# Performance work log

Hardware: AMD Instinct MI355X
Metric: run time of the kernel (lower is better)

## Reference

```python
import jax, jax.numpy as jnp
from jax import lax
import numpy as np

IMG = 1024          # original image H = W
HD = WD = 256       # detection feature map (stride 4)
CD = 128            # detection feature channels
HS = WS = 512       # segmentation feature map (stride 2)
CS = 32             # segmentation feature channels
FC = 1024           # detection head conv / fc filters
K = 2000            # pre-NMS topk
MAX_OUT = 500       # max proposals after NMS
NMS_THR = 1.0       # distance threshold in detection-grid units
CROP = 48           # instance crop size (instance_crop_size // 2)
CI = 64             # instance conv channels


def _conv(x, w, b):
    # x: [H,W,Cin] single map -> same-padded conv
    y = lax.conv_general_dilated(x[None], w, (1, 1), 'SAME',
                                 dimension_numbers=('NHWC', 'HWIO', 'NHWC'))[0]
    return y + b


def _conv_b(x, w, b):
    # x: [N,H,W,Cin] batched conv
    y = lax.conv_general_dilated(x, w, (1, 1), 'SAME',
                                 dimension_numbers=('NHWC', 'HWIO', 'NHWC'))
    return y + b


def setup_inputs() -> dict:
    key = jax.random.key(0)
    ks = jax.random.split(key, 10)
    s = 0.02
    return {
        'detection_features': jax.random.normal(ks[0], (HD, WD, CD), jnp.float32),
        'segmentation_features': jax.random.normal(ks[1], (HS, WS, CS), jnp.float32),
        'Wc': jax.random.normal(ks[2], (3, 3, CD, FC), jnp.float32) * s,
        'bc': jnp.zeros((FC,), jnp.float32),
        'Wfc': jax.random.normal(ks[3], (1, 1, FC, FC), jnp.float32) * s,
        'bfc': jnp.zeros((FC,), jnp.float32),
        'Ws': jax.random.normal(ks[4], (1, 1, FC, 1), jnp.float32) * s,
        'bs': jnp.zeros((1,), jnp.float32),
        'Wr': jax.random.normal(ks[5], (1, 1, FC, 2), jnp.float32) * s,
        'br': jnp.zeros((2,), jnp.float32),
        'Wi': jax.random.normal(ks[6], (3, 3, CS, CI), jnp.float32) * s,
        'bi': jnp.zeros((CI,), jnp.float32),
        'Wo': jax.random.normal(ks[7], (3, 3, CI, 1), jnp.float32) * s,
        'bo': jnp.zeros((1,), jnp.float32),
    }


def _forward(detection_features, segmentation_features,
             Wc, bc, Wfc, bfc, Ws, bs, Wr, br, Wi, bi, Wo, bo):
    x = jax.nn.relu(_conv(detection_features, Wc, bc))
    x = jax.nn.relu(_conv(x, Wfc, bfc))
    scores = jax.nn.sigmoid(_conv(x, Ws, bs))[..., 0]          # [HD,WD]
    reg = _conv(x, Wr, br)                                      # [HD,WD,2] offsets in grid units

    # ---- proposal_locations: decode, topk, distance-threshold NMS ----
    yy, xx = jnp.meshgrid(jnp.arange(HD, dtype=jnp.float32),
                          jnp.arange(WD, dtype=jnp.float32), indexing='ij')
    ctr = jnp.stack([yy, xx], axis=-1) + 0.5                    # cell centers
    locs = (ctr + reg) / jnp.array([HD, WD], jnp.float32)       # normalized [0,1]
    flat_scores = scores.reshape(-1)                            # [HD*WD]
    flat_locs = locs.reshape(-1, 2)

    top_s, top_i = lax.top_k(flat_scores, K)                    # pre-NMS topk (sorted desc)
    cand = flat_locs[top_i]                                     # [K,2] normalized

    grid_xy = cand * jnp.array([HD, WD], jnp.float32)           # grid-unit coords
    d2 = jnp.sum((grid_xy[:, None, :] - grid_xy[None, :, :]) ** 2, axis=-1)  # [K,K]
    close = d2 < (NMS_THR * NMS_THR)
    later = jnp.arange(K)[None, :] > jnp.arange(K)[:, None]

    def nms_body(i, suppressed):
        keep_i = jnp.logical_not(suppressed[i])
        return suppressed | (keep_i & close[i] & later[i])

    suppressed = lax.fori_loop(0, K, nms_body, jnp.zeros((K,), jnp.bool_))
    masked = jnp.where(suppressed, -1.0, top_s)
    proposed_scores, sel = lax.top_k(masked, MAX_OUT)           # [500]
    sel_norm = cand[sel]                                        # [500,2]
    decoded = sel_norm * jnp.float32(IMG)                       # pixel coords

    # ---- instance head: crop stride-2 seg features around each proposal ----
    seg_loc = decoded / 2.0
    start = jnp.clip(jnp.round(seg_loc - CROP / 2), 0, HS - CROP).astype(jnp.int32)  # [500,2]

    def crop_one(st):
        return lax.dynamic_slice(segmentation_features, (st[0], st[1], 0), (CROP, CROP, CS))

    crops = jax.vmap(crop_one)(start)                           # [500,48,48,CS]
    h = jax.nn.relu(_conv_b(crops, Wi, bi))                     # [500,48,48,CI]
    instance_output = jax.nn.sigmoid(_conv_b(h, Wo, bo))        # [500,48,48,1]

    cy, cx = jnp.meshgrid(jnp.arange(CROP), jnp.arange(CROP), indexing='ij')
    instance_coords = start[:, None, None, :] + jnp.stack([cy, cx], axis=-1)[None]  # [500,48,48,2]

    return proposed_scores, decoded, instance_output, instance_coords


def reference(detection_features, segmentation_features,
              Wc, bc, Wfc, bfc, Ws, bs, Wr, br, Wi, bi, Wo, bo):
    return _forward(detection_features, segmentation_features,
                    Wc, bc, Wfc, bfc, Ws, bs, Wr, br, Wi, bi, Wo, bo)
```

## Files before the change

kernel.cpp:

```cpp
#include <hip/hip_runtime.h>
#include <math.h>

#define KTOP 2000
#define MAXOUT 500
#define CANDCAP 4096
#define NSEL 3600
#define RC2 16

typedef __attribute__((ext_vector_type(8))) short short8;
typedef __attribute__((ext_vector_type(4))) float f32x4;
typedef __attribute__((ext_vector_type(4))) double f64x4;

__device__ __forceinline__ unsigned short f2bf(float f) {
  unsigned int u = __float_as_uint(f);
  unsigned int r = ((u >> 16) & 1u) + 0x7FFFu;
  return (unsigned short)((u + r) >> 16);
}

__global__ __launch_bounds__(256) void transpose_bf16_kernel(
    const float* __restrict__ W, unsigned short* __restrict__ WT, int K, int N)
{
  __shared__ float t[32][33];
  const int k0 = blockIdx.x << 5, n0 = blockIdx.y << 5;
  const int tid = threadIdx.x;
  const int r = tid >> 5, c = tid & 31;
#pragma unroll
  for (int p = 0; p < 4; ++p)
    t[r + (p << 3)][c] = W[(size_t)(k0 + r + (p << 3)) * N + n0 + c];
  __syncthreads();
#pragma unroll
  for (int p = 0; p < 4; ++p)
    WT[(size_t)(n0 + r + (p << 3)) * K + k0 + c] = f2bf(t[c][r + (p << 3)]);
}

__global__ __launch_bounds__(256) void prep_wib_kernel(
    const float* __restrict__ Wi, unsigned short* __restrict__ WiB)
{
  const int t = blockIdx.x * 256 + threadIdx.x;
  if (t < 9 * 64 * 32) {
    const int tap = t / 2048, r = t & 2047, co = r >> 5, ci = r & 31;
    WiB[t] = f2bf(Wi[((size_t)tap * 32 + ci) * 64 + co]);
  }
}

__global__ __launch_bounds__(256) void pad_df_bf16(
    const float* __restrict__ df, unsigned short* __restrict__ dfb)
{
  const int t = blockIdx.x * 256 + threadIdx.x;
  if (t >= 258 * 258 * 16) return;
  const int p = t >> 4;
  const int c8 = (t & 15) << 3;
  const int gy = p / 258 - 1, gx = p % 258 - 1;
  uint4 out = make_uint4(0, 0, 0, 0);
  if (gy >= 0 && gy < 256 && gx >= 0 && gx < 256) {
    const float* src = &df[((size_t)(gy * 256 + gx)) * 128 + c8];
    const float4 v0 = *(const float4*)src;
    const float4 v1 = *(const float4*)(src + 4);
    out.x = (unsigned int)f2bf(v0.x) | ((unsigned int)f2bf(v0.y) << 16);
    out.y = (unsigned int)f2bf(v0.z) | ((unsigned int)f2bf(v0.w) << 16);
    out.z = (unsigned int)f2bf(v1.x) | ((unsigned int)f2bf(v1.y) << 16);
    out.w = (unsigned int)f2bf(v1.z) | ((unsigned int)f2bf(v1.w) << 16);
  }
  *(uint4*)&dfb[(size_t)p * 128 + c8] = out;
}

__global__ __launch_bounds__(256) void conv1_mfma(
    const unsigned short* __restrict__ dfb, const unsigned short* __restrict__ WcT,
    const float* __restrict__ bc, unsigned short* __restrict__ x1b, int pt0)
{
  __shared__ __align__(16) unsigned short smem[2 * 128 * 64];
  unsigned short* As = smem;
  unsigned short* Bs = smem + 128 * 64;
  const int tid = threadIdx.x;
  const int n0 = blockIdx.x << 7;
  const int m0 = blockIdx.y << 7;
  const int Pbase = (pt0 << 6) + m0;
  const int ybase = Pbase >> 8, x0 = Pbase & 255;
  const int wv = tid >> 6, lane = tid & 63;
  const int wm = (wv & 1) << 6, wn = (wv >> 1) << 6;
  const int l15 = lane & 15, quad = lane >> 4;

  const int tr = tid >> 3;
  const int g8 = tid & 7;
  const int xg = ((g8 ^ (tr & 7)) << 4);
  int koff[2];
#pragma unroll
  for (int s = 0; s < 2; ++s)
    koff[s] = ((((s << 2) + quad) ^ (l15 & 7)) << 3);

  f32x4 acc[4][4];
  const f32x4 z4 = {0.f, 0.f, 0.f, 0.f};
#pragma unroll
  for (int i = 0; i < 4; ++i)
#pragma unroll
    for (int j = 0; j < 4; ++j) acc[i][j] = z4;

  for (int kc = 0; kc < 18; ++kc) {
    const int tap = kc >> 1, ci0 = (kc & 1) << 6;
    const int dy = tap / 3 - 1, dx = tap % 3 - 1;
    const size_t abase =
        ((size_t)((ybase + dy + 1) * 258 + (x0 + dx + 1))) * 128 + ci0;
#pragma unroll
    for (int p = 0; p < 4; ++p) {
      const int r = (p << 5) + tr;
      __builtin_amdgcn_global_load_lds(
          (const unsigned int*)((const char*)&dfb[abase + (size_t)r * 128] + xg),
          (unsigned int*)&As[(r << 6) + (g8 << 3)], 16, 0, 0);
    }
#pragma unroll
    for (int p = 0; p < 4; ++p) {
      const int n = (p << 5) + tr;
      __builtin_amdgcn_global_load_lds(
          (const unsigned int*)((const char*)&WcT[(size_t)(n0 + n) * 1152 + (kc << 6)] + xg),
          (unsigned int*)&Bs[(n << 6) + (g8 << 3)], 16, 0, 0);
    }
    __syncthreads();
#pragma unroll
    for (int s = 0; s < 2; ++s) {
      short8 a[4], b[4];
#pragma unroll
      for (int i = 0; i < 4; ++i)
        a[i] = *(short8*)&As[((wm + (i << 4) + l15) << 6) + koff[s]];
#pragma unroll
      for (int j = 0; j < 4; ++j)
        b[j] = *(short8*)&Bs[((wn + (j << 4) + l15) << 6) + koff[s]];
#pragma unroll
      for (int i = 0; i < 4; ++i)
#pragma unroll
        for (int j = 0; j < 4; ++j)
          acc[i][j] = __builtin_amdgcn_mfma_f32_16x16x32_bf16(a[i], b[j], acc[i][j], 0, 0, 0);
    }
    __syncthreads();
  }
#pragma unroll
  for (int i = 0; i < 4; ++i)
#pragma unroll
    for (int j = 0; j < 4; ++j) {
      const int col = wn + (j << 4) + l15;
      const float bb = bc[n0 + col];
#pragma unroll
      for (int rg = 0; rg < 4; ++rg) {
        const int row = wm + (i << 4) + (quad << 2) + rg;
        const float v = fmaxf(acc[i][j][rg] + bb, 0.f);
        x1b[(size_t)(m0 + row) * 1024 + n0 + col] = f2bf(v);
      }
    }
}

__global__ __launch_bounds__(256) void fc_mfma(
    const unsigned short* __restrict__ x1b, const unsigned short* __restrict__ WfcT,
    const float* __restrict__ bfc, const float* __restrict__ Wsc,
    float* __restrict__ part, int pt0)
{
  __shared__ __align__(16) unsigned short smem[2 * 128 * 64];
  unsigned short* As = smem;
  unsigned short* Bs = smem + 128 * 64;
  const int tid = threadIdx.x;
  const int n0 = blockIdx.x << 7;
  const int m0 = blockIdx.y << 7;
  const int Pbase = (pt0 << 6) + m0;
  const int wv = tid >> 6, lane = tid & 63;
  const int wm = (wv & 1) << 6, wn = (wv >> 1) << 6;
  const int l15 = lane & 15, quad = lane >> 4;

  const int tr = tid >> 3;
  const int g8 = tid & 7;
  const int xg = ((g8 ^ (tr & 7)) << 4);
  int koff[2];
#pragma unroll
  for (int s = 0; s < 2; ++s)
    koff[s] = ((((s << 2) + quad) ^ (l15 & 7)) << 3);

  f32x4 acc[4][4];
  const f32x4 z4 = {0.f, 0.f, 0.f, 0.f};
#pragma unroll
  for (int i = 0; i < 4; ++i)
#pragma unroll
    for (int j = 0; j < 4; ++j) acc[i][j] = z4;

  for (int kc = 0; kc < 16; ++kc) {
#pragma unroll
    for (int p = 0; p < 4; ++p) {
      const int r = (p << 5) + tr;
      __builtin_amdgcn_global_load_lds(
          (const unsigned int*)((const char*)&x1b[(size_t)(m0 + r) * 1024 + (kc << 6)] + xg),
          (unsigned int*)&As[(r << 6) + (g8 << 3)], 16, 0, 0);
    }
#pragma unroll
    for (int p = 0; p < 4; ++p) {
      const int n = (p << 5) + tr;
      __builtin_amdgcn_global_load_lds(
          (const unsigned int*)((const char*)&WfcT[(size_t)(n0 + n) * 1024 + (kc << 6)] + xg),
          (unsigned int*)&Bs[(n << 6) + (g8 << 3)], 16, 0, 0);
    }
    __syncthreads();
#pragma unroll
    for (int s = 0; s < 2; ++s) {
      short8 a[4], b[4];
#pragma unroll
      for (int i = 0; i < 4; ++i)
        a[i] = *(short8*)&As[((wm + (i << 4) + l15) << 6) + koff[s]];
#pragma unroll
      for (int j = 0; j < 4; ++j)
        b[j] = *(short8*)&Bs[((wn + (j << 4) + l15) << 6) + koff[s]];
#pragma unroll
      for (int i = 0; i < 4; ++i)
#pragma unroll
        for (int j = 0; j < 4; ++j)
          acc[i][j] = __builtin_amdgcn_mfma_f32_16x16x32_bf16(a[i], b[j], acc[i][j], 0, 0, 0);
    }
    __syncthreads();
  }
  float wsv[4], bfv[4];
#pragma unroll
  for (int j = 0; j < 4; ++j) {
    const int col = n0 + wn + (j << 4) + l15;
    wsv[j] = Wsc[col];
    bfv[j] = bfc[col];
  }
  float* red = (float*)smem;
#pragma unroll
  for (int i = 0; i < 4; ++i)
#pragma unroll
    for (int rg = 0; rg < 4; ++rg) {
      const int row = wm + (i << 4) + (quad << 2) + rg;
      float ps = 0.f;
#pragma unroll
      for (int j = 0; j < 4; ++j) {
        const float v = fmaxf(acc[i][j][rg] + bfv[j], 0.f);
        ps = fmaf(v, wsv[j], ps);
      }
      red[row * 33 + ((wv >> 1) << 4) + l15] = ps;
    }
  __syncthreads();
  if (tid < 128) {
    float s = 0.f;
#pragma unroll
    for (int sl = 0; sl < 32; ++sl) s += red[tid * 33 + sl];
    part[(size_t)blockIdx.x * 65536 + Pbase + tid] = s;
  }
}

__global__ __launch_bounds__(256) void head_finalize_kernel(
    const float* __restrict__ part, const float* __restrict__ bs,
    float* __restrict__ scores)
{
  const int pix = blockIdx.x * 256 + threadIdx.x;
  float s = 0.f;
#pragma unroll
  for (int cb = 0; cb < 8; ++cb) s += part[(size_t)cb * 65536 + pix];
  s += bs[0];
  scores[pix] = 1.f / (1.f + expf(-s));
}

__global__ __launch_bounds__(1024) void select_kernel(
    const float* __restrict__ scores, unsigned int* __restrict__ cand_idx,
    unsigned int* __restrict__ cand_cnt)
{
  __shared__ unsigned int hist[256];
  __shared__ unsigned int sh_prefix;
  __shared__ int scan_s[1024];
  const int tid = threadIdx.x;

  unsigned int prefix = 0u;
  int need = NSEL;
  for (int byte = 3; byte >= 0; --byte) {
    if (tid < 256) hist[tid] = 0u;
    __syncthreads();
    const int sh = byte * 8;
    const unsigned int mhi = (byte == 3) ? 0u : (0xFFFFFFFFu << (sh + 8));
    for (int i = tid; i < 65536; i += 1024) {
      const unsigned int b = __float_as_uint(scores[i]);
      if ((b & mhi) == prefix) atomicAdd(&hist[(b >> sh) & 255u], 1u);
    }
    __syncthreads();
    if (tid == 0) {
      int cum = 0;
      for (int v = 255; v >= 0; --v) {
        const int c = (int)hist[v];
        if (cum + c >= need) { sh_prefix = prefix | ((unsigned)v << sh); break; }
        cum += c;
      }
      hist[0] = (unsigned int)cum;
    }
    __syncthreads();
    prefix = sh_prefix;
    need -= (int)hist[0];
    __syncthreads();
  }
  const float thr = __uint_as_float(prefix);

  const int b0 = tid << 6;
  int my = 0;
  for (int k = 0; k < 64; ++k)
    if (scores[b0 + k] >= thr) ++my;
  scan_s[tid] = my;
  __syncthreads();
  for (int off = 1; off < 1024; off <<= 1) {
    const int a = scan_s[tid];
    const int b = (tid >= off) ? scan_s[tid - off] : 0;
    __syncthreads();
    scan_s[tid] = a + b;
    __syncthreads();
  }
  int pos = scan_s[tid] - my;
  const int total = scan_s[1023];
  for (int k = 0; k < 64; ++k) {
    if (scores[b0 + k] >= thr) {
      if (pos < CANDCAP) cand_idx[pos] = (unsigned int)(b0 + k);
      ++pos;
    }
  }
  if (tid == 0)
    *cand_cnt = (unsigned int)(total > CANDCAP ? CANDCAP : total);
}

#define PSTR 133
__global__ __launch_bounds__(512) void rescore_conv(
    const float* __restrict__ df, const float* __restrict__ Wc,
    const float* __restrict__ bc,
    const unsigned int* __restrict__ cand_idx,
    const unsigned int* __restrict__ cand_cnt,
    double* __restrict__ x1g)
{
  __shared__ double patt[16 * PSTR];
  __shared__ int rrs[16], ccs[16];
  const int cnt = (int)*cand_cnt;
  const int c0 = blockIdx.x * RC2;
  if (c0 >= cnt) return;
  const int tid = threadIdx.x;
  const int wv = tid >> 6, lane = tid & 63;
  const int m = lane & 15, quad = lane >> 4;
  const int co_base = wv << 7;

  if (tid < 16) {
    const int slot = (c0 + tid < cnt) ? c0 + tid : c0;
    const unsigned int idx = cand_idx[slot];
    rrs[tid] = (int)(idx >> 8); ccs[tid] = (int)(idx & 255u);
  }

  f64x4 acc[8];
  const f64x4 z4 = {0.0, 0.0, 0.0, 0.0};
#pragma unroll
  for (int t = 0; t < 8; ++t) acc[t] = z4;

  for (int tap = 0; tap < 9; ++tap) {
    const int dy = tap / 3 - 1, dx = tap % 3 - 1;
    __syncthreads();
    for (int p = tid; p < 2048; p += 512) {
      const int c = p >> 7, ci = p & 127;
      const int gy = rrs[c] + dy, gx = ccs[c] + dx;
      float v = 0.f;
      if (gy >= 0 && gy < 256 && gx >= 0 && gx < 256)
        v = df[((size_t)((gy << 8) + gx)) * 128 + ci];
      patt[c * PSTR + ci] = (double)v;
    }
    __syncthreads();
    const float* wrow = &Wc[(size_t)(tap * 128 + quad) * 1024 + co_base + m];
    float wf[8];
#pragma unroll
    for (int t = 0; t < 8; ++t) wf[t] = wrow[t << 4];
    for (int k4 = 0; k4 < 32; ++k4) {
      float wn[8];
      if (k4 + 1 < 32) {
#pragma unroll
        for (int t = 0; t < 8; ++t)
          wn[t] = wrow[(size_t)((k4 + 1) << 2) * 1024 + (t << 4)];
      }
      const double a = patt[m * PSTR + (k4 << 2) + quad];
#pragma unroll
      for (int t = 0; t < 8; ++t)
        acc[t] = __builtin_amdgcn_mfma_f64_16x16x4f64(a, (double)wf[t], acc[t], 0, 0, 0);
      if (k4 + 1 < 32) {
#pragma unroll
        for (int t = 0; t < 8; ++t) wf[t] = wn[t];
      }
    }
  }
#pragma unroll
  for (int t = 0; t < 8; ++t) {
    const int co = co_base + (t << 4) + m;
    const double bb = (double)bc[co];
#pragma unroll
    for (int rg = 0; rg < 4; ++rg) {
      const int cand = (quad << 2) + rg;
      if (c0 + cand < cnt) {
        const double v = acc[t][rg] + bb;
        x1g[(size_t)(c0 + cand) * 1024 + co] = v > 0.0 ? v : 0.0;
      }
    }
  }
}

__global__ __launch_bounds__(512) void rescore_fc(
    const double* __restrict__ x1g, const float* __restrict__ Wfc,
    const float* __restrict__ bfc, const float* __restrict__ Wsc,
    const float* __restrict__ bs, const float* __restrict__ Wrg,
    const float* __restrict__ br,
    const unsigned int* __restrict__ cand_cnt,
    unsigned long long* __restrict__ cand_sb,
    double* __restrict__ cand_ry, double* __restrict__ cand_rx)
{
  __shared__ double xbuf[16 * PSTR];
  __shared__ double partw[3][8][16];
  const int cnt = (int)*cand_cnt;
  const int c0 = blockIdx.x * RC2;
  if (c0 >= cnt) return;
  const int tid = threadIdx.x;
  const int wv = tid >> 6, lane = tid & 63;
  const int m = lane & 15, quad = lane >> 4;
  const int co_base = wv << 7;

  f64x4 acc[8];
  const f64x4 z4 = {0.0, 0.0, 0.0, 0.0};
#pragma unroll
  for (int t = 0; t < 8; ++t) acc[t] = z4;

  for (int kc = 0; kc < 8; ++kc) {
    __syncthreads();
    for (int p = tid; p < 2048; p += 512) {
      const int c = p >> 7, k = p & 127;
      const int row = (c0 + c < cnt) ? c0 + c : c0;
      xbuf[c * PSTR + k] = x1g[(size_t)row * 1024 + (kc << 7) + k];
    }
    __syncthreads();
    const float* wrow = &Wfc[(size_t)((kc << 7) + quad) * 1024 + co_base + m];
    float wf[8];
#pragma unroll
    for (int t = 0; t < 8; ++t) wf[t] = wrow[t << 4];
    for (int k4 = 0; k4 < 32; ++k4) {
      float wn[8];
      if (k4 + 1 < 32) {
#pragma unroll
        for (int t = 0; t < 8; ++t)
          wn[t] = wrow[(size_t)((k4 + 1) << 2) * 1024 + (t << 4)];
      }
      const double a = xbuf[m * PSTR + (k4 << 2) + quad];
#pragma unroll
      for (int t = 0; t < 8; ++t)
        acc[t] = __builtin_amdgcn_mfma_f64_16x16x4f64(a, (double)wf[t], acc[t], 0, 0, 0);
      if (k4 + 1 < 32) {
#pragma unroll
        for (int t = 0; t < 8; ++t) wf[t] = wn[t];
      }
    }
  }

  double ps[4] = {0, 0, 0, 0}, py[4] = {0, 0, 0, 0}, px[4] = {0, 0, 0, 0};
#pragma unroll
  for (int t = 0; t < 8; ++t) {
    const int co = co_base + (t << 4) + m;
    const double bfv = (double)bfc[co];
    const double wsv = (double)Wsc[co];
    const double w0 = (double)Wrg[co * 2], w1 = (double)Wrg[co * 2 + 1];
#pragma unroll
    for (int rg = 0; rg < 4; ++rg) {
      double v = acc[t][rg] + bfv;
      v = v > 0.0 ? v : 0.0;
      ps[rg] = fma(v, wsv, ps[rg]);
      py[rg] = fma(v, w0, py[rg]);
      px[rg] = fma(v, w1, px[rg]);
    }
  }
#pragma unroll
  for (int off = 1; off <= 8; off <<= 1) {
#pragma unroll
    for (int rg = 0; rg < 4; ++rg) {
      ps[rg] += __shfl_xor(ps[rg], off, 64);
      py[rg] += __shfl_xor(py[rg], off, 64);
      px[rg] += __shfl_xor(px[rg], off, 64);
    }
  }
  if (m == 0) {
#pragma unroll
    for (int rg = 0; rg < 4; ++rg) {
      const int cand = (quad << 2) + rg;
      partw[0][wv][cand] = ps[rg];
      partw[1][wv][cand] = py[rg];
      partw[2][wv][cand] = px[rg];
    }
  }
  __syncthreads();
  if (tid < 48) {
    const int cand = tid & 15, h = tid >> 4;
    double s = 0.0;
#pragma unroll
    for (int w8 = 0; w8 < 8; ++w8) s += partw[h][w8][cand];
    if (c0 + cand < cnt) {
      if (h == 0) {
        const double lg = s + (double)bs[0];
        const double sg = 1.0 / (1.0 + exp(-lg));
        cand_sb[c0 + cand] = (unsigned long long)__double_as_longlong(sg);
      } else if (h == 1) cand_ry[c0 + cand] = s + (double)br[0];
      else               cand_rx[c0 + cand] = s + (double)br[1];
    }
  }
}

__global__ __launch_bounds__(1024) void proposal_kernel(
    const unsigned int* __restrict__ cand_idx,
    const unsigned int* __restrict__ cand_cnt,
    const unsigned long long* __restrict__ cand_sb,
    const double* __restrict__ cand_ry, const double* __restrict__ cand_rx,
    unsigned int* __restrict__ cellrank, unsigned int* __restrict__ nbrg,
    double* __restrict__ cyg, double* __restrict__ cxg,
    int* __restrict__ startb, float* __restrict__ out_ps,
    float* __restrict__ out_dec)
{
  __shared__ unsigned long long sk[2048];
  __shared__ unsigned int si[2048];
  __shared__ unsigned int hist[256];
  __shared__ unsigned long long sh_pref;
  __shared__ unsigned char kept[2048];
  __shared__ unsigned char nbrc[2048];
  __shared__ int scan[2048];
  __shared__ volatile unsigned int changed;
  __shared__ int sh_maxreg;

  const int tid = threadIdx.x;
  const int cnt = (int)*cand_cnt;

  for (int i = tid; i < 65536; i += 1024) cellrank[i] = 0xFFFFFFFFu;

  unsigned long long prefix = 0ull;
  int need = KTOP;
  for (int byte = 7; byte >= 0; --byte) {
    if (tid < 256) hist[tid] = 0u;
    __syncthreads();
    const int sh = byte * 8;
    const unsigned long long mhi =
        (byte == 7) ? 0ull : (0xFFFFFFFFFFFFFFFFull << (sh + 8));
    for (int i = tid; i < cnt; i += 1024) {
      const unsigned long long k = cand_sb[i];
      if ((k & mhi) == prefix) atomicAdd(&hist[(unsigned int)((k >> sh) & 255u)], 1u);
    }
    __syncthreads();
    if (tid == 0) {
      int cum = 0;
      for (int v = 255; v >= 0; --v) {
        const int c = (int)hist[v];
        if (cum + c >= need) {
          sh_pref = prefix | ((unsigned long long)(unsigned)v << sh);
          break;
        }
// ... 227 lines not shown
      b[j] = *(const short8*)&WiB[((tap << 6) + (j << 4) + l15) * 32 + (quad << 3)];
#pragma unroll
    for (int i = 0; i < 6; ++i) {
      const short8 a = *(const short8*)&ins[(pbase[i] + off) * ISTR + (quad << 3)];
#pragma unroll
      for (int j = 0; j < 4; ++j)
        acc[i][j] = __builtin_amdgcn_mfma_f32_16x16x32_bf16(a, b[j], acc[i][j], 0, 0, 0);
    }
  }

  float bv[4];
#pragma unroll
  for (int j = 0; j < 4; ++j) bv[j] = bi[(j << 4) + l15];

  for (int half = 0; half < 2; ++half) {
    __syncthreads();
    if ((wv >> 1) == half) {
#pragma unroll
      for (int i = 0; i < 6; ++i)
#pragma unroll
        for (int j = 0; j < 4; ++j)
#pragma unroll
          for (int rg = 0; rg < 4; ++rg) {
            const int m = wmb + (i << 4) + (quad << 2) + rg;
            const int pp = m - half * 192;
            const float v = fmaxf(acc[i][j][rg] + bv[j], 0.f);
            ins[pp * 72 + (j << 4) + l15] = f2bf(v);
          }
    }
    __syncthreads();
    for (int t = tid; t < 192 * 8; t += 256) {
      const int pp = t >> 3, c8 = t & 7;
      const uint4 v = *(const uint4*)&ins[pp * 72 + (c8 << 3)];
      *(uint4*)&h[((size_t)li * 2304 + (tile * 384 + half * 192 + pp)) * 64 + (c8 << 3)] = v;
    }
  }
}

__global__ __launch_bounds__(256) void conv_o_kernel(
    const unsigned short* __restrict__ h, const float* __restrict__ Wo,
    const float* __restrict__ bo, const int* __restrict__ startb,
    float* __restrict__ out_io, float* __restrict__ out_ic, int inst0)
{
  __shared__ __align__(16) unsigned short hs[324 * 72];
  __shared__ float wos[576];
  const int li = blockIdx.y;
  const int inst = inst0 + li;
  const int tile = blockIdx.x;
  const int ty0 = (tile / 3) << 4;
  const int tx0 = (tile % 3) << 4;
  const int tid = threadIdx.x;

  for (int i = tid; i < 576; i += 256) wos[i] = Wo[i];
  for (int p = tid; p < 324; p += 256) {
    const int iy = p / 18, ix = p - iy * 18;
    const int gy = ty0 - 1 + iy, gx = tx0 - 1 + ix;
    unsigned short* dst = &hs[p * 72];
    if (gy >= 0 && gy < 48 && gx >= 0 && gx < 48) {
      const unsigned short* src = &h[((size_t)li * 2304 + gy * 48 + gx) * 64];
#pragma unroll
      for (int q = 0; q < 8; ++q) *(uint4*)&dst[q << 3] = *(const uint4*)&src[q << 3];
    } else {
#pragma unroll
      for (int q = 0; q < 8; ++q) *(uint4*)&dst[q << 3] = make_uint4(0, 0, 0, 0);
    }
  }
  __syncthreads();

  const int ly = tid >> 4, lx = tid & 15;
  float a = 0.f;
#pragma unroll
  for (int ky = 0; ky < 3; ++ky)
#pragma unroll
    for (int kx = 0; kx < 3; ++kx) {
      const unsigned short* hp = &hs[((ly + ky) * 18 + lx + kx) * 72];
      const float* wp = &wos[(ky * 3 + kx) << 6];
#pragma unroll
      for (int c8 = 0; c8 < 8; ++c8) {
        const uint4 hv = *(const uint4*)&hp[c8 << 3];
        const unsigned int uu[4] = {hv.x, hv.y, hv.z, hv.w};
#pragma unroll
        for (int e = 0; e < 4; ++e) {
          const float f0 = __uint_as_float(uu[e] << 16);
          const float f1 = __uint_as_float(uu[e] & 0xFFFF0000u);
          a = fmaf(f0, wp[(c8 << 3) + (e << 1)], a);
          a = fmaf(f1, wp[(c8 << 3) + (e << 1) + 1], a);
        }
      }
    }
  a += bo[0];
  const float o = 1.f / (1.f + expf(-a));
  const int gy = ty0 + ly, gx = tx0 + lx;
  const size_t p = ((size_t)inst * 48 + gy) * 48 + gx;
  out_io[p] = o;
  const int sy = startb[inst * 2], sx = startb[inst * 2 + 1];
  out_ic[p * 2]     = (float)(sy + gy);
  out_ic[p * 2 + 1] = (float)(sx + gx);
}

extern "C" void kernel_launch(void* const* d_in, const int* in_sizes, int n_in,
                              void* d_out, int out_size, void* d_ws, size_t ws_size,
                              hipStream_t stream)
{
  const float* df  = (const float*)d_in[0];
  const float* seg = (const float*)d_in[1];
  const float* Wc  = (const float*)d_in[2];
  const float* bc  = (const float*)d_in[3];
  const float* Wfc = (const float*)d_in[4];
  const float* bfc = (const float*)d_in[5];
  const float* Wsc = (const float*)d_in[6];
  const float* bs  = (const float*)d_in[7];
  const float* Wrg = (const float*)d_in[8];
  const float* br  = (const float*)d_in[9];
  const float* Wi  = (const float*)d_in[10];
  const float* bi  = (const float*)d_in[11];
  const float* Wo  = (const float*)d_in[12];
  const float* bo  = (const float*)d_in[13];

  const size_t SZ_WCT = 2359296ull, SZ_WFT = 2097152ull, SZ_WIB = 36864ull,
               SZ_DFB = 17040384ull,
               SZ_PART = 2097152ull, SZ_SC = 262144ull, SZ_CR = 262144ull,
               SZ_NB = 131072ull, SZ_STB = 4096ull, SZ_CI = CANDCAP * 4ull,
               SZ_SB = CANDCAP * 8ull, SZ_RY = CANDCAP * 8ull,
               SZ_RX = CANDCAP * 8ull, SZ_CY = 16384ull, SZ_CX = 16384ull,
               SZ_X1G = (size_t)CANDCAP * 1024ull * 8ull,
               SZ_CNT = 256ull;
  const size_t FIXED = SZ_WCT + SZ_WFT + SZ_WIB + SZ_DFB + SZ_PART + SZ_SC +
                       SZ_CR + SZ_NB + SZ_STB + SZ_CI + SZ_SB + SZ_RY + SZ_RX +
                       SZ_CY + SZ_CX + SZ_X1G + SZ_CNT;
  char* w = (char*)d_ws;
  size_t region = (ws_size > FIXED) ? ((ws_size - FIXED) & ~(size_t)255) : 0;
  char* fb = w + region;
  unsigned short* WcT = (unsigned short*)fb;   fb += SZ_WCT;
  unsigned short* WfcT = (unsigned short*)fb;  fb += SZ_WFT;
  unsigned short* WiB = (unsigned short*)fb;   fb += SZ_WIB;
  unsigned short* dfb = (unsigned short*)fb;   fb += SZ_DFB;
  float* part = (float*)fb;                    fb += SZ_PART;
  float* scores = (float*)fb;                  fb += SZ_SC;
  unsigned int* cellrank = (unsigned int*)fb;  fb += SZ_CR;
  unsigned int* nbrg = (unsigned int*)fb;      fb += SZ_NB;
  int* startb = (int*)fb;                      fb += SZ_STB;
  unsigned int* cand_idx = (unsigned int*)fb;  fb += SZ_CI;
  unsigned long long* cand_sb = (unsigned long long*)fb; fb += SZ_SB;
  double* cand_ry = (double*)fb;               fb += SZ_RY;
  double* cand_rx = (double*)fb;               fb += SZ_RX;
  double* cyg = (double*)fb;                   fb += SZ_CY;
  double* cxg = (double*)fb;                   fb += SZ_CX;
  double* x1g = (double*)fb;                   fb += SZ_X1G;
  unsigned int* cand_cnt = (unsigned int*)fb;
  unsigned short* x1b = (unsigned short*)w;
  unsigned short* hb = (unsigned short*)w;

  size_t tiles_fit = region / 131072ull;
  int pt_chunk = 2;
  while ((size_t)(pt_chunk * 2) <= tiles_fit && pt_chunk < 1024) pt_chunk <<= 1;
  size_t inst_fit = region / 294912ull;
  const int opts[12] = {500, 250, 125, 100, 50, 25, 20, 10, 5, 4, 2, 1};
  int inst_chunk = 1;
  for (int o = 0; o < 12; ++o)
    if ((size_t)opts[o] <= inst_fit) { inst_chunk = opts[o]; break; }

  float* out = (float*)d_out;
  float* out_ps  = out;
  float* out_dec = out + 500;
  float* out_io  = out + 1500;
  float* out_ic  = out + 1153500;

  transpose_bf16_kernel<<<dim3(36, 32), 256, 0, stream>>>(Wc, WcT, 1152, 1024);
  transpose_bf16_kernel<<<dim3(32, 32), 256, 0, stream>>>(Wfc, WfcT, 1024, 1024);
  prep_wib_kernel<<<72, 256, 0, stream>>>(Wi, WiB);
  pad_df_bf16<<<4161, 256, 0, stream>>>(df, dfb);

  for (int c = 0; c < 1024 / pt_chunk; ++c) {
    conv1_mfma<<<dim3(8, pt_chunk / 2), 256, 0, stream>>>(dfb, WcT, bc, x1b,
                                                          c * pt_chunk);
    fc_mfma<<<dim3(8, pt_chunk / 2), 256, 0, stream>>>(x1b, WfcT, bfc, Wsc,
                                                       part, c * pt_chunk);
  }
  head_finalize_kernel<<<256, 256, 0, stream>>>(part, bs, scores);
  select_kernel<<<1, 1024, 0, stream>>>(scores, cand_idx, cand_cnt);
  rescore_conv<<<CANDCAP / RC2, 512, 0, stream>>>(df, Wc, bc, cand_idx,
                                                  cand_cnt, x1g);
  rescore_fc<<<CANDCAP / RC2, 512, 0, stream>>>(x1g, Wfc, bfc, Wsc, bs, Wrg,
                                                br, cand_cnt, cand_sb,
                                                cand_ry, cand_rx);
  proposal_kernel<<<1, 1024, 0, stream>>>(cand_idx, cand_cnt, cand_sb, cand_ry,
                                          cand_rx, cellrank, nbrg, cyg, cxg,
                                          startb, out_ps, out_dec);
  for (int c = 0; c < 500 / inst_chunk; ++c) {
    conv_i_mfma<<<dim3(6, inst_chunk), 256, 0, stream>>>(seg, WiB, bi, startb,
                                                         hb, c * inst_chunk);
    conv_o_kernel<<<dim3(9, inst_chunk), 256, 0, stream>>>(hb, Wo, bo, startb,
                                                           out_io, out_ic,
                                                           c * inst_chunk);
  }
}
```

Measured before the change: 1.354 ms.

## Use 256x256 double-buffered MFMA GEMM tiles with phased compute and wider rescore

The conv1 and fc GEMMs move from 128x128 tiles with 256 threads to 256x256 tiles with 512 threads. Global-to-LDS loads are double-buffered and the MFMA work is split into barrier-separated phases with s_setprio, so loads overlap compute and each tile reuses more data. The fc epilogue now reduces with wave shuffles, and the number of partial-score slices drops from 8 to 4. rescore_conv now handles 32 candidates per block split across two column halves. The larger tiles use much more LDS and registers, which lowers occupancy, and they need a larger minimum chunk size.

Result: faster. 1.282 ms (-5.3%).

```diff
diff --git a/kernel.cpp b/kernel.cpp
--- a/kernel.cpp
+++ b/kernel.cpp
@@ -5,6 +5,7 @@
 #define MAXOUT 500
 #define CANDCAP 4096
 #define NSEL 3600
+#define RCC 32
 #define RC2 16
 
 typedef __attribute__((ext_vector_type(8))) short short8;
@@ -15,6 +16,19 @@
   unsigned int u = __float_as_uint(f);
   unsigned int r = ((u >> 16) & 1u) + 0x7FFFu;
   return (unsigned short)((u + r) >> 16);
+}
+
+__device__ __forceinline__ void ld_lds16(const void* g, void* l) {
+  __builtin_amdgcn_global_load_lds((const unsigned int*)g, (unsigned int*)l,
+                                   16, 0, 0);
+}
+
+__device__ __forceinline__ void hard_barrier() {
+  asm volatile("" ::: "memory");
+  __builtin_amdgcn_sched_barrier(0);
+  __builtin_amdgcn_s_barrier();
+  __builtin_amdgcn_sched_barrier(0);
+  asm volatile("" ::: "memory");
 }
 
 __global__ __launch_bounds__(256) void transpose_bf16_kernel(
@@ -64,179 +78,247 @@
   *(uint4*)&dfb[(size_t)p * 128 + c8] = out;
 }
 
-__global__ __launch_bounds__(256) void conv1_mfma(
+__device__ __forceinline__ void ktile_phases(
+    const unsigned short* __restrict__ A0, const unsigned short* __restrict__ B0,
+    const int arow, const int brow, const int ok0, const int ok1,
+    f32x4 (&acc)[8][4])
+{
+  short8 Af[4][2], Bf[2][2][2];
+#pragma unroll
+  for (int m = 0; m < 4; ++m) {
+    Af[m][0] = *(const short8*)&A0[((arow + (m << 4)) << 6) + ok0];
+    Af[m][1] = *(const short8*)&A0[((arow + (m << 4)) << 6) + ok1];
+  }
+#pragma unroll
+  for (int n = 0; n < 2; ++n) {
+    Bf[0][n][0] = *(const short8*)&B0[((brow + (n << 4)) << 6) + ok0];
+    Bf[0][n][1] = *(const short8*)&B0[((brow + (n << 4)) << 6) + ok1];
+  }
+  hard_barrier();
+  __builtin_amdgcn_s_setprio(1);
+#pragma unroll
+  for (int m = 0; m < 4; ++m)
+#pragma unroll
+    for (int n = 0; n < 2; ++n) {
+      acc[m][n] = __builtin_amdgcn_mfma_f32_16x16x32_bf16(Af[m][0], Bf[0][n][0], acc[m][n], 0, 0, 0);
+      acc[m][n] = __builtin_amdgcn_mfma_f32_16x16x32_bf16(Af[m][1], Bf[0][n][1], acc[m][n], 0, 0, 0);
+    }
+  __builtin_amdgcn_s_setprio(0);
+  hard_barrier();
+#pragma unroll
+  for (int n = 0; n < 2; ++n) {
+    Bf[1][n][0] = *(const short8*)&B0[((brow + ((n + 2) << 4)) << 6) + ok0];
+    Bf[1][n][1] = *(const short8*)&B0[((brow + ((n + 2) << 4)) << 6) + ok1];
+  }
+  hard_barrier();
+  __builtin_amdgcn_s_setprio(1);
+#pragma unroll
+  for (int m = 0; m < 4; ++m)
+#pragma unroll
+    for (int n = 0; n < 2; ++n) {
+      acc[m][n + 2] = __builtin_amdgcn_mfma_f32_16x16x32_bf16(Af[m][0], Bf[1][n][0], acc[m][n + 2], 0, 0, 0);
+      acc[m][n + 2] = __builtin_amdgcn_mfma_f32_16x16x32_bf16(Af[m][1], Bf[1][n][1], acc[m][n + 2], 0, 0, 0);
+    }
+  __builtin_amdgcn_s_setprio(0);
+  hard_barrier();
+#pragma unroll
+  for (int m = 0; m < 4; ++m) {
+    Af[m][0] = *(const short8*)&A0[((arow + 64 + (m << 4)) << 6) + ok0];
+    Af[m][1] = *(const short8*)&A0[((arow + 64 + (m << 4)) << 6) + ok1];
+  }
+  hard_barrier();
+  __builtin_amdgcn_s_setprio(1);
+#pragma unroll
+  for (int m = 0; m < 4; ++m)
+#pragma unroll
+    for (int n = 0; n < 2; ++n) {
+      acc[m + 4][n + 2] = __builtin_amdgcn_mfma_f32_16x16x32_bf16(Af[m][0], Bf[1][n][0], acc[m + 4][n + 2], 0, 0, 0);
+      acc[m + 4][n + 2] = __builtin_amdgcn_mfma_f32_16x16x32_bf16(Af[m][1], Bf[1][n][1], acc[m + 4][n + 2], 0, 0, 0);
+    }
+  __builtin_amdgcn_s_setprio(0);
+  hard_barrier();
+  __builtin_amdgcn_s_setprio(1);
+#pragma unroll
+  for (int m = 0; m < 4; ++m)
+#pragma unroll
+    for (int n = 0; n < 2; ++n) {
+      acc[m + 4][n] = __builtin_amdgcn_mfma_f32_16x16x32_bf16(Af[m][0], Bf[0][n][0], acc[m + 4][n], 0, 0, 0);
+      acc[m + 4][n] = __builtin_amdgcn_mfma_f32_16x16x32_bf16(Af[m][1], Bf[0][n][1], acc[m + 4][n], 0, 0, 0);
+    }
+  __builtin_amdgcn_s_setprio(0);
+  hard_barrier();
+}
+
+__global__ __launch_bounds__(512) void conv1_mfma(
     const unsigned short* __restrict__ dfb, const unsigned short* __restrict__ WcT,
     const float* __restrict__ bc, unsigned short* __restrict__ x1b, int pt0)
 {
-  __shared__ __align__(16) unsigned short smem[2 * 128 * 64];
-  unsigned short* As = smem;
-  unsigned short* Bs = smem + 128 * 64;
+  __shared__ __align__(16) unsigned short smem[65536];
   const int tid = threadIdx.x;
-  const int n0 = blockIdx.x << 7;
-  const int m0 = blockIdx.y << 7;
-  const int Pbase = (pt0 << 6) + m0;
-  const int ybase = Pbase >> 8, x0 = Pbase & 255;
   const int wv = tid >> 6, lane = tid & 63;
-  const int wm = (wv & 1) << 6, wn = (wv >> 1) << 6;
+  const int wr = wv >> 2, wc = wv & 3;
   const int l15 = lane & 15, quad = lane >> 4;
-
-  const int tr = tid >> 3;
-  const int g8 = tid & 7;
+  const int n0 = blockIdx.x << 8;
+  const int lm0 = blockIdx.y << 8;
+  const int Pbase = (pt0 << 6) + lm0;
+  const int y = Pbase >> 8;
+  const int tr = tid >> 3, g8 = tid & 7;
   const int xg = ((g8 ^ (tr & 7)) << 4);
-  int koff[2];
-#pragma unroll
-  for (int s = 0; s < 2; ++s)
-    koff[s] = ((((s << 2) + quad) ^ (l15 & 7)) << 3);
-
-  f32x4 acc[4][4];
+  const int axr = l15 & 7;
+  const int ok0 = ((quad ^ axr) << 3);
+  const int ok1 = (((4 + quad) ^ axr) << 3);
+  const int arow = (wr << 7) + l15;
+  const int brow = (wc << 6) + l15;
+
+  float bcv[4];
+#pragma unroll
+  for (int j = 0; j < 4; ++j) bcv[j] = bc[n0 + (wc << 6) + (j << 4) + l15];
+
+  f32x4 acc[8][4];
   const f32x4 z4 = {0.f, 0.f, 0.f, 0.f};
 #pragma unroll
-  for (int i = 0; i < 4; ++i)
+  for (int i = 0; i < 8; ++i)
 #pragma unroll
     for (int j = 0; j < 4; ++j) acc[i][j] = z4;
 
-  for (int kc = 0; kc < 18; ++kc) {
-    const int tap = kc >> 1, ci0 = (kc & 1) << 6;
+  const char* WB = (const char*)WcT + ((size_t)(n0 + tr) * 1152) * 2 + xg;
+  unsigned short* lA = &smem[(tr << 6) + (g8 << 3)];
+
+  auto issue = [&](int kt, int buf) {
+    const int tap = kt >> 1, ci0 = (kt & 1) << 6;
     const int dy = tap / 3 - 1, dx = tap % 3 - 1;
-    const size_t abase =
-        ((size_t)((ybase + dy + 1) * 258 + (x0 + dx + 1))) * 128 + ci0;
-#pragma unroll
-    for (int p = 0; p < 4; ++p) {
-      const int r = (p << 5) + tr;
-      __builtin_amdgcn_global_load_lds(
-          (const unsigned int*)((const char*)&dfb[abase + (size_t)r * 128] + xg),
-          (unsigned int*)&As[(r << 6) + (g8 << 3)], 16, 0, 0);
-    }
-#pragma unroll
-    for (int p = 0; p < 4; ++p) {
-      const int n = (p << 5) + tr;
-      __builtin_amdgcn_global_load_lds(
-          (const unsigned int*)((const char*)&WcT[(size_t)(n0 + n) * 1152 + (kc << 6)] + xg),
-          (unsigned int*)&Bs[(n << 6) + (g8 << 3)], 16, 0, 0);
-    }
-    __syncthreads();
-#pragma unroll
-    for (int s = 0; s < 2; ++s) {
-      short8 a[4], b[4];
-#pragma unroll
-      for (int i = 0; i < 4; ++i)
-        a[i] = *(short8*)&As[((wm + (i << 4) + l15) << 6) + koff[s]];
-#pragma unroll
-      for (int j = 0; j < 4; ++j)
-        b[j] = *(short8*)&Bs[((wn + (j << 4) + l15) << 6) + koff[s]];
-#pragma unroll
-      for (int i = 0; i < 4; ++i)
-#pragma unroll
-        for (int j = 0; j < 4; ++j)
-          acc[i][j] = __builtin_amdgcn_mfma_f32_16x16x32_bf16(a[i], b[j], acc[i][j], 0, 0, 0);
-    }
-    __syncthreads();
-  }
-#pragma unroll
-  for (int i = 0; i < 4; ++i)
-#pragma unroll
-    for (int j = 0; j < 4; ++j) {
-      const int col = wn + (j << 4) + l15;
-      const float bb = bc[n0 + col];
+    const char* Ab = (const char*)dfb +
+        (((size_t)((y + dy + 1) * 258 + dx + 1)) * 128 + ci0) * 2 +
+        (size_t)tr * 256 + xg;
+    unsigned short* la = lA + buf * 32768;
+    unsigned short* lb = la + 16384;
+    const char* Bb = WB + (size_t)kt * 128;
+#pragma unroll
+    for (int i = 0; i < 4; ++i)
+      ld_lds16(Ab + (size_t)i * 16384, la + i * 4096);
+#pragma unroll
+    for (int i = 0; i < 4; ++i)
+      ld_lds16(Bb + (size_t)i * 147456, lb + i * 4096);
+  };
+
+  issue(0, 0);
+  issue(1, 1);
+#pragma unroll 2
+  for (int kt = 0; kt < 18; ++kt) {
+    const int buf = kt & 1;
+    if (kt < 17) asm volatile("s_waitcnt vmcnt(8)" ::: "memory");
+    else         asm volatile("s_waitcnt vmcnt(0)" ::: "memory");
+    hard_barrier();
+    ktile_phases(&smem[buf * 32768], &smem[buf * 32768 + 16384],
+                 arow, brow, ok0, ok1, acc);
+    if (kt < 16) issue(kt + 2, buf);
+  }
+
+#pragma unroll
+  for (int m = 0; m < 8; ++m)
+#pragma unroll
+    for (int n = 0; n < 4; ++n) {
+      const int col = n0 + (wc << 6) + (n << 4) + l15;
+      const float bb = bcv[n];
 #pragma unroll
       for (int rg = 0; rg < 4; ++rg) {
-        const int row = wm + (i << 4) + (quad << 2) + rg;
-        const float v = fmaxf(acc[i][j][rg] + bb, 0.f);
-        x1b[(size_t)(m0 + row) * 1024 + n0 + col] = f2bf(v);
-      }
-    }
-}
-
-__global__ __launch_bounds__(256) void fc_mfma(
+        const int row = lm0 + (wr << 7) + (m << 4) + (quad << 2) + rg;
+        const float v = fmaxf(acc[m][n][rg] + bb, 0.f);
+        x1b[(size_t)row * 1024 + col] = f2bf(v);
+      }
+    }
+}
+
+__global__ __launch_bounds__(512) void fc_mfma(
     const unsigned short* __restrict__ x1b, const unsigned short* __restrict__ WfcT,
     const float* __restrict__ bfc, const float* __restrict__ Wsc,
     float* __restrict__ part, int pt0)
 {
-  __shared__ __align__(16) unsigned short smem[2 * 128 * 64];
-  unsigned short* As = smem;
-  unsigned short* Bs = smem + 128 * 64;
+  __shared__ __align__(16) unsigned short smem[65536];
   const int tid = threadIdx.x;
-  const int n0 = blockIdx.x << 7;
-  const int m0 = blockIdx.y << 7;
-  const int Pbase = (pt0 << 6) + m0;
   const int wv = tid >> 6, lane = tid & 63;
-  const int wm = (wv & 1) << 6, wn = (wv >> 1) << 6;
+  const int wr = wv >> 2, wc = wv & 3;
   const int l15 = lane & 15, quad = lane >> 4;
-
-  const int tr = tid >> 3;
-  const int g8 = tid & 7;
+  const int n0 = blockIdx.x << 8;
+  const int lm0 = blockIdx.y << 8;
+  const int Pbase = (pt0 << 6) + lm0;
+  const int tr = tid >> 3, g8 = tid & 7;
   const int xg = ((g8 ^ (tr & 7)) << 4);
-  int koff[2];
-#pragma unroll
-  for (int s = 0; s < 2; ++s)
-    koff[s] = ((((s << 2) + quad) ^ (l15 & 7)) << 3);
-
-  f32x4 acc[4][4];
-  const f32x4 z4 = {0.f, 0.f, 0.f, 0.f};
-#pragma unroll
-  for (int i = 0; i < 4; ++i)
-#pragma unroll
-    for (int j = 0; j < 4; ++j) acc[i][j] = z4;
-
-  for (int kc = 0; kc < 16; ++kc) {
-#pragma unroll
-    for (int p = 0; p < 4; ++p) {
-      const int r = (p << 5) + tr;
-      __builtin_amdgcn_global_load_lds(
-          (const unsigned int*)((const char*)&x1b[(size_t)(m0 + r) * 1024 + (kc << 6)] + xg),
-          (unsigned int*)&As[(r << 6) + (g8 << 3)], 16, 0, 0);
-    }
-#pragma unroll
-    for (int p = 0; p < 4; ++p) {
-      const int n = (p << 5) + tr;
-      __builtin_amdgcn_global_load_lds(
-          (const unsigned int*)((const char*)&WfcT[(size_t)(n0 + n) * 1024 + (kc << 6)] + xg),
-          (unsigned int*)&Bs[(n << 6) + (g8 << 3)], 16, 0, 0);
-    }
-    __syncthreads();
-#pragma unroll
-    for (int s = 0; s < 2; ++s) {
-      short8 a[4], b[4];
-#pragma unroll
-      for (int i = 0; i < 4; ++i)
-        a[i] = *(short8*)&As[((wm + (i << 4) + l15) << 6) + koff[s]];
-#pragma unroll
-      for (int j = 0; j < 4; ++j)
-        b[j] = *(short8*)&Bs[((wn + (j << 4) + l15) << 6) + koff[s]];
-#pragma unroll
-      for (int i = 0; i < 4; ++i)
-#pragma unroll
-        for (int j = 0; j < 4; ++j)
-          acc[i][j] = __builtin_amdgcn_mfma_f32_16x16x32_bf16(a[i], b[j], acc[i][j], 0, 0, 0);
-    }
-    __syncthreads();
-  }
+  const int axr = l15 & 7;
+  const int ok0 = ((quad ^ axr) << 3);
+  const int ok1 = (((4 + quad) ^ axr) << 3);
+  const int arow = (wr << 7) + l15;
+  const int brow = (wc << 6) + l15;
+
   float wsv[4], bfv[4];
 #pragma unroll
   for (int j = 0; j < 4; ++j) {
-    const int col = n0 + wn + (j << 4) + l15;
+    const int col = n0 + (wc << 6) + (j << 4) + l15;
     wsv[j] = Wsc[col];
     bfv[j] = bfc[col];
   }
+
+  f32x4 acc[8][4];
+  const f32x4 z4 = {0.f, 0.f, 0.f, 0.f};
+#pragma unroll
+  for (int i = 0; i < 8; ++i)
+#pragma unroll
+    for (int j = 0; j < 4; ++j) acc[i][j] = z4;
+
+  const char* AB = (const char*)x1b + ((size_t)(lm0 + tr) * 1024) * 2 + xg;
+  const char* WB = (const char*)WfcT + ((size_t)(n0 + tr) * 1024) * 2 + xg;
+  unsigned short* lA = &smem[(tr << 6) + (g8 << 3)];
+
+  auto issue = [&](int kt, int buf) {
+    unsigned short* la = lA + buf * 32768;
+    unsigned short* lb = la + 16384;
+    const char* Ab = AB + (size_t)kt * 128;
+    const char* Bb = WB + (size_t)kt * 128;
+#pragma unroll
+    for (int i = 0; i < 4; ++i)
+      ld_lds16(Ab + (size_t)i * 131072, la + i * 4096);
+#pragma unroll
+    for (int i = 0; i < 4; ++i)
+      ld_lds16(Bb + (size_t)i * 131072, lb + i * 4096);
+  };
+
+  issue(0, 0);
+  issue(1, 1);
+#pragma unroll 2
+  for (int kt = 0; kt < 16; ++kt) {
+    const int buf = kt & 1;
+    if (kt < 15) asm volatile("s_waitcnt vmcnt(8)" ::: "memory");
+    else         asm volatile("s_waitcnt vmcnt(0)" ::: "memory");
+    hard_barrier();
+    ktile_phases(&smem[buf * 32768], &smem[buf * 32768 + 16384],
+                 arow, brow, ok0, ok1, acc);
+    if (kt < 14) issue(kt + 2, buf);
+  }
+
   float* red = (float*)smem;
 #pragma unroll
-  for (int i = 0; i < 4; ++i)
+  for (int m = 0; m < 8; ++m)
 #pragma unroll
     for (int rg = 0; rg < 4; ++rg) {
-      const int row = wm + (i << 4) + (quad << 2) + rg;
       float ps = 0.f;
 #pragma unroll
-      for (int j = 0; j < 4; ++j) {
-        const float v = fmaxf(acc[i][j][rg] + bfv[j], 0.f);
-        ps = fmaf(v, wsv[j], ps);
-      }
-      red[row * 33 + ((wv >> 1) << 4) + l15] = ps;
-    }
-  __syncthreads();
-  if (tid < 128) {
+      for (int n = 0; n < 4; ++n) {
+        const float v = fmaxf(acc[m][n][rg] + bfv[n], 0.f);
+        ps = fmaf(v, wsv[n], ps);
+      }
+#pragma unroll
+      for (int off = 1; off <= 8; off <<= 1)
+        ps += __shfl_xor(ps, off, 64);
+      if (l15 == 0) {
+        const int row = (wr << 7) + (m << 4) + (quad << 2) + rg;
+        red[row * 5 + wc] = ps;
+      }
+    }
+  __syncthreads();
+  if (tid < 256) {
     float s = 0.f;
 #pragma unroll
-    for (int sl = 0; sl < 32; ++sl) s += red[tid * 33 + sl];
+    for (int w8 = 0; w8 < 4; ++w8) s += red[tid * 5 + w8];
     part[(size_t)blockIdx.x * 65536 + Pbase + tid] = s;
   }
 }
@@ -248,7 +330,7 @@
   const int pix = blockIdx.x * 256 + threadIdx.x;
   float s = 0.f;
 #pragma unroll
-  for (int cb = 0; cb < 8; ++cb) s += part[(size_t)cb * 65536 + pix];
+  for (int cb = 0; cb < 4; ++cb) s += part[(size_t)cb * 65536 + pix];
   s += bs[0];
   scores[pix] = 1.f / (1.f + expf(-s));
 }
@@ -323,31 +405,34 @@
     const unsigned int* __restrict__ cand_cnt,
     double* __restrict__ x1g)
 {
-  __shared__ double patt[16 * PSTR];
-  __shared__ int rrs[16], ccs[16];
+  __shared__ double patt[RCC * PSTR];
+  __shared__ int rrs[RCC], ccs[RCC];
   const int cnt = (int)*cand_cnt;
-  const int c0 = blockIdx.x * RC2;
+  const int nb = blockIdx.x & 1;
+  const int c0 = (blockIdx.x >> 1) * RCC;
   if (c0 >= cnt) return;
   const int tid = threadIdx.x;
   const int wv = tid >> 6, lane = tid & 63;
   const int m = lane & 15, quad = lane >> 4;
-  const int co_base = wv << 7;
-
-  if (tid < 16) {
+  const int co_base = (nb << 9) + (wv << 6);
+
+  if (tid < RCC) {
     const int slot = (c0 + tid < cnt) ? c0 + tid : c0;
     const unsigned int idx = cand_idx[slot];
     rrs[tid] = (int)(idx >> 8); ccs[tid] = (int)(idx & 255u);
   }
 
-  f64x4 acc[8];
+  f64x4 acc[2][4];
   const f64x4 z4 = {0.0, 0.0, 0.0, 0.0};
 #pragma unroll
-  for (int t = 0; t < 8; ++t) acc[t] = z4;
+  for (int ct = 0; ct < 2; ++ct)
+#pragma unroll
+    for (int t = 0; t < 4; ++t) acc[ct][t] = z4;
 
   for (int tap = 0; tap < 9; ++tap) {
     const int dy = tap / 3 - 1, dx = tap % 3 - 1;
     __syncthreads();
-    for (int p = tid; p < 2048; p += 512) {
+    for (int p = tid; p < RCC * 128; p += 512) {
       const int c = p >> 7, ci = p & 127;
       const int gy = rrs[c] + dy, gx = ccs[c] + dx;
       float v = 0.f;
@@ -357,39 +442,45 @@
     }
     __syncthreads();
     const float* wrow = &Wc[(size_t)(tap * 128 + quad) * 1024 + co_base + m];
-    float wf[8];
-#pragma unroll
-    for (int t = 0; t < 8; ++t) wf[t] = wrow[t << 4];
+    float wf[4];
+#pragma unroll
+    for (int t = 0; t < 4; ++t) wf[t] = wrow[t << 4];
     for (int k4 = 0; k4 < 32; ++k4) {
-      float wn[8];
+      float wn[4];
       if (k4 + 1 < 32) {
 #pragma unroll
-        for (int t = 0; t < 8; ++t)
+        for (int t = 0; t < 4; ++t)
           wn[t] = wrow[(size_t)((k4 + 1) << 2) * 1024 + (t << 4)];
       }
-      const double a = patt[m * PSTR + (k4 << 2) + quad];
-#pragma unroll
-      for (int t = 0; t < 8; ++t)
-        acc[t] = __builtin_amdgcn_mfma_f64_16x16x4f64(a, (double)wf[t], acc[t], 0, 0, 0);
+      const double a0 = patt[m * PSTR + (k4 << 2) + quad];
+      const double a1 = patt[(16 + m) * PSTR + (k4 << 2) + quad];
+#pragma unroll
+      for (int t = 0; t < 4; ++t)
+        acc[0][t] = __builtin_amdgcn_mfma_f64_16x16x4f64(a0, (double)wf[t], acc[0][t], 0, 0, 0);
+#pragma unroll
+      for (int t = 0; t < 4; ++t)
+        acc[1][t] = __builtin_amdgcn_mfma_f64_16x16x4f64(a1, (double)wf[t], acc[1][t], 0, 0, 0);
       if (k4 + 1 < 32) {
 #pragma unroll
-        for (int t = 0; t < 8; ++t) wf[t] = wn[t];
-      }
-    }
-  }
-#pragma unroll
-  for (int t = 0; t < 8; ++t) {
-    const int co = co_base + (t << 4) + m;
-    const double bb = (double)bc[co];
-#pragma unroll
-    for (int rg = 0; rg < 4; ++rg) {
-      const int cand = (quad << 2) + rg;
-      if (c0 + cand < cnt) {
-        const double v = acc[t][rg] + bb;
-        x1g[(size_t)(c0 + cand) * 1024 + co] = v > 0.0 ? v : 0.0;
-      }
-    }
-  }
+        for (int t = 0; t < 4; ++t) wf[t] = wn[t];
+      }
+    }
+  }
+#pragma unroll
+  for (int ct = 0; ct < 2; ++ct)
+#pragma unroll
+    for (int t = 0; t < 4; ++t) {
+      const int co = co_base + (t << 4) + m;
+      const double bb = (double)bc[co];
+#pragma unroll
+      for (int rg = 0; rg < 4; ++rg) {
+        const int cand = (ct << 4) + (quad << 2) + rg;
+        if (c0 + cand < cnt) {
+          const double v = acc[ct][t][rg] + bb;
+          x1g[(size_t)(c0 + cand) * 1024 + co] = v > 0.0 ? v : 0.0;
+        }
+      }
+    }
 }
 
 __global__ __launch_bounds__(512) void rescore_fc(
@@ -923,7 +1014,7 @@
   unsigned short* hb = (unsigned short*)w;
 
   size_t tiles_fit = region / 131072ull;
-  int pt_chunk = 2;
+  int pt_chunk = 4;
   while ((size_t)(pt_chunk * 2) <= tiles_fit && pt_chunk < 1024) pt_chunk <<= 1;
   size_t inst_fit = region / 294912ull;
   const int opts[12] = {500, 250, 125, 100, 50, 25, 20, 10, 5, 4, 2, 1};
@@ -943,15 +1034,15 @@
   pad_df_bf16<<<4161, 256, 0, stream>>>(df, dfb);
 
   for (int c = 0; c < 1024 / pt_chunk; ++c) {
-    conv1_mfma<<<dim3(8, pt_chunk / 2), 256, 0, stream>>>(dfb, WcT, bc, x1b,
+    conv1_mfma<<<dim3(4, pt_chunk / 4), 512, 0, stream>>>(dfb, WcT, bc, x1b,
                                                           c * pt_chunk);
-    fc_mfma<<<dim3(8, pt_chunk / 2), 256, 0, stream>>>(x1b, WfcT, bfc, Wsc,
+    fc_mfma<<<dim3(4, pt_chunk / 4), 512, 0, stream>>>(x1b, WfcT, bfc, Wsc,
                                                        part, c * pt_chunk);
   }
   head_finalize_kernel<<<256, 256, 0, stream>>>(part, bs, scores);
   select_kernel<<<1, 1024, 0, stream>>>(scores, cand_idx, cand_cnt);
-  rescore_conv<<<CANDCAP / RC2, 512, 0, stream>>>(df, Wc, bc, cand_idx,
-                                                  cand_cnt, x1g);
+  rescore_conv<<<(CANDCAP / RCC) * 2, 512, 0, stream>>>(df, Wc, bc, cand_idx,
+                                                        cand_cnt, x1g);
   rescore_fc<<<CANDCAP / RC2, 512, 0, stream>>>(x1g, Wfc, bfc, Wsc, bs, Wrg,
                                                 br, cand_cnt, cand_sb,
                                                 cand_ry, cand_rx);
```
